# Kernel tuning notes

Measured on AMD Instinct MI355X. Metric: run time of the kernel, lower is better.

Reference implementation:

```python
import jax, jax.numpy as jnp
import numpy as np

N_BASIS = 128   # n_atom_basis F
N_INT   = 3     # n_interactions
N_RBF   = 20
CUTOFF  = 5.0
MAX_Z   = 100
EPS     = 1e-8
N_ATOMS = 25000
N_EDGES = 200000


def setup_inputs() -> dict:
    key = jax.random.key(0)
    ks = jax.random.split(key, 16)
    F = N_BASIS
    s = 0.02
    z     = jax.random.randint(ks[0], (N_ATOMS,), 1, MAX_Z)
    pos   = jax.random.uniform(ks[1], (N_ATOMS, 3), dtype=jnp.float32) * 2.0  # small box -> inside cutoff
    idx_i = jax.random.randint(ks[2], (N_EDGES,), 0, N_ATOMS)
    idx_j = jax.random.randint(ks[3], (N_EDGES,), 0, N_ATOMS)
    emb   = jax.random.normal(ks[4], (MAX_Z, F), dtype=jnp.float32) * s
    fW    = jax.random.normal(ks[5], (N_RBF, 3 * F * N_INT), dtype=jnp.float32) * s
    fb    = jnp.zeros((3 * F * N_INT,), jnp.float32)
    iW1   = jax.random.normal(ks[6], (N_INT, F, F), dtype=jnp.float32) * s
    ib1   = jnp.zeros((N_INT, F), jnp.float32)
    iW2   = jax.random.normal(ks[7], (N_INT, F, 3 * F), dtype=jnp.float32) * s
    ib2   = jnp.zeros((N_INT, 3 * F), jnp.float32)
    mWmix = jax.random.normal(ks[8], (N_INT, F, 2 * F), dtype=jnp.float32) * s
    mW1   = jax.random.normal(ks[9], (N_INT, 2 * F, F), dtype=jnp.float32) * s
    mb1   = jnp.zeros((N_INT, F), jnp.float32)
    mW2   = jax.random.normal(ks[10], (N_INT, F, 3 * F), dtype=jnp.float32) * s
    mb2   = jnp.zeros((N_INT, 3 * F), jnp.float32)
    return dict(z=z, pos=pos, idx_i=idx_i, idx_j=idx_j, emb=emb, fW=fW, fb=fb,
                iW1=iW1, ib1=ib1, iW2=iW2, ib2=ib2,
                mWmix=mWmix, mW1=mW1, mb1=mb1, mW2=mW2, mb2=mb2)


def reference(z, pos, idx_i, idx_j, emb, fW, fb, iW1, ib1, iW2, ib2,
              mWmix, mW1, mb1, mW2, mb2):
    F = N_BASIS
    n_atoms = z.shape[0]
    # geometry
    r_ij = pos[idx_j] - pos[idx_i]                                  # [E,3]
    r_ij = jnp.where(jnp.abs(r_ij) < 1e-6, 1e-6, r_ij)
    d_ij = jnp.linalg.norm(r_ij, axis=1, keepdims=True)             # [E,1]
    dir_ij = r_ij / d_ij                                            # [E,3]
    # Gaussian radial basis
    offsets = jnp.linspace(0.0, CUTOFF, N_RBF)
    width = offsets[1] - offsets[0]
    coeff = -0.5 / (width * width)
    phi = jnp.exp(coeff * (d_ij[..., None] - offsets) ** 2)         # [E,1,n_rbf]
    # cosine cutoff
    fcut = 0.5 * (jnp.cos(jnp.pi * d_ij / CUTOFF) + 1.0) * (d_ij < CUTOFF)  # [E,1]
    filters = (phi @ fW + fb) * fcut[..., None]                     # [E,1,3F*I]
    filter_list = jnp.split(filters, N_INT, axis=-1)                # each [E,1,3F]
    # initial atom features
    q = emb[z][:, None, :]                                          # [N,1,F]
    mu = jnp.zeros((n_atoms, 3, F), q.dtype)                        # [N,3,F]
    for t in range(N_INT):
        # --- interaction (gather - filter-multiply - scatter-add) ---
        x = jax.nn.silu(q @ iW1[t] + ib1[t]) @ iW2[t] + ib2[t]      # [N,1,3F]
        xj = x[idx_j]                                               # [E,1,3F]
        muj = mu[idx_j]                                             # [E,3,F]
        x = filter_list[t] * xj                                     # [E,1,3F]
        dq, dmuR, dmumu = jnp.split(x, 3, axis=-1)                  # [E,1,F] each
        dq = jax.ops.segment_sum(dq, idx_i, num_segments=n_atoms)   # [N,1,F]
        dmu = dmuR * dir_ij[..., None] + dmumu * muj                # [E,3,F]
        dmu = jax.ops.segment_sum(dmu, idx_i, num_segments=n_atoms) # [N,3,F]
        q = q + dq
        mu = mu + dmu
        # --- mixing (intra-atomic) ---
        mu_mix = mu @ mWmix[t]                                      # [N,3,2F]
        mu_V, mu_W = jnp.split(mu_mix, 2, axis=-1)                  # [N,3,F]
        mu_Vn = jnp.sqrt(jnp.sum(mu_V ** 2, axis=-2, keepdims=True) + EPS)  # [N,1,F]
        ctx = jnp.concatenate([q, mu_Vn], axis=-1)                  # [N,1,2F]
        x = jax.nn.silu(ctx @ mW1[t] + mb1[t]) @ mW2[t] + mb2[t]    # [N,1,3F]
        dq_intra, dmu_intra, dqmu_intra = jnp.split(x, 3, axis=-1)
        dmu_intra = dmu_intra * mu_W                                # [N,3,F]
        dqmu_intra = dqmu_intra * jnp.sum(mu_V * mu_W, axis=1, keepdims=True)
        q = q + dq_intra + dqmu_intra
        mu = mu + dmu_intra
    return q.squeeze(1), mu
```

## Files before the change

### kernel.cpp

```cpp
#include <hip/hip_runtime.h>
#include <hip/hip_bf16.h>

#define F 128
#define F3 384
#define NRBF 20
#define NITER 3

typedef __hip_bfloat16 bf16;
typedef __bf16 bfrag __attribute__((ext_vector_type(8)));
typedef float f32x4 __attribute__((ext_vector_type(4)));

__device__ __forceinline__ float b2f(bf16 v) { return __bfloat162float(v); }
__device__ __forceinline__ bf16 f2b(float v) { return __float2bfloat16(v); }
__device__ __forceinline__ bfrag ldb(const bf16* p) { return *(const bfrag*)p; }
__device__ __forceinline__ bfrag ldsb(const __bf16* p) { return *(const bfrag*)p; }
__device__ __forceinline__ bfrag cvtf(const float* p) {
    bfrag r;
#pragma unroll
    for (int j = 0; j < 8; ++j) r[j] = (__bf16)p[j];
    return r;
}

__global__ void detect_kernel(const unsigned short* __restrict__ raw, int n_u16,
                              int* __restrict__ flag) {
    int i = blockIdx.x * blockDim.x + threadIdx.x;
    int bad = 0;
    for (int k = i; k < n_u16; k += blockDim.x * gridDim.x) {
        unsigned e = (raw[k] >> 7) & 0xFFu;
        if (e >= 140u) bad = 1;
    }
    if (bad) atomicOr(flag, 1);
}

__global__ void cvt_dual_kernel(const void* __restrict__ src, float* __restrict__ dst,
                                int n, const int* __restrict__ flag) {
    int i = blockIdx.x * blockDim.x + threadIdx.x;
    if (i >= n) return;
    if (*flag) dst[i] = ((const float*)src)[i];
    else       dst[i] = b2f(((const bf16*)src)[i]);
}

__global__ void transpose_bf16_kernel(const float* __restrict__ src, bf16* __restrict__ dst,
                                      int K, int Nn, int total) {
    int i = blockIdx.x * blockDim.x + threadIdx.x;
    if (i >= total) return;
    int slice = K * Nn;
    int t = i / slice, j = i - t * slice;
    int n = j / K, k = j - n * K;
    dst[i] = f2b(src[t * slice + k * Nn + n]);
}

__global__ void fwt_kernel(const float* __restrict__ fW, const float* __restrict__ fb,
                           bf16* __restrict__ dst, int total) {
    int idx = blockIdx.x * blockDim.x + threadIdx.x;
    if (idx >= total) return;
    int k = idx & 31, rest = idx >> 5;
    int n = rest % F3, t = rest / F3;
    float v = (k < NRBF) ? fW[k * (F3 * NITER) + t * F3 + n]
                         : (k == NRBF ? fb[t * F3 + n] : 0.0f);
    dst[idx] = f2b(v);
}

__global__ void geom_kernel(const float* __restrict__ pos, const int* __restrict__ ii,
                            const int* __restrict__ jj, const int* __restrict__ rank,
                            bf16* __restrict__ phifc2, float* __restrict__ dir2,
                            int* __restrict__ jj2, int E) {
    int e = blockIdx.x * blockDim.x + threadIdx.x;
    if (e >= E) return;
    int i = ii[e], j = jj[e], l = rank[e];
    float r[3];
#pragma unroll
    for (int d = 0; d < 3; ++d) {
        float v = pos[j * 3 + d] - pos[i * 3 + d];
        if (fabsf(v) < 1e-6f) v = 1e-6f;
        r[d] = v;
    }
    float dd = sqrtf(r[0] * r[0] + r[1] * r[1] + r[2] * r[2]);
    float inv = 1.0f / dd;
    jj2[l] = j;
#pragma unroll
    for (int d = 0; d < 3; ++d) dir2[(size_t)l * 4 + d] = r[d] * inv;
    dir2[(size_t)l * 4 + 3] = 0.0f;
    const float CUT = 5.0f;
    const float PI = 3.14159265358979323846f;
    float fc = (dd < CUT) ? 0.5f * (cosf(PI * dd / CUT) + 1.0f) : 0.0f;
    const float width = CUT / (NRBF - 1);
    const float coeff = -0.5f / (width * width);
    bf16* pr = phifc2 + (size_t)l * 32;
#pragma unroll
    for (int k = 0; k < NRBF; ++k) {
        float diff = dd - (float)k * width;
        pr[k] = f2b(expf(coeff * diff * diff) * fc);
    }
    pr[NRBF] = f2b(fc);
#pragma unroll
    for (int k = NRBF + 1; k < 32; ++k) pr[k] = f2b(0.0f);
}

__global__ void embed_kernel(const int* __restrict__ z, const float* __restrict__ emb,
                             float* __restrict__ q, int N) {
    int idx = blockIdx.x * blockDim.x + threadIdx.x;
    if (idx >= N * F) return;
    int n = idx >> 7, f = idx & 127;
    q[idx] = emb[z[n] * F + f];
}

__global__ void count_kernel(const int* __restrict__ ii, int* __restrict__ counts, int E) {
    int e = blockIdx.x * blockDim.x + threadIdx.x;
    if (e < E) atomicAdd(&counts[ii[e]], 1);
}

__global__ void scan_kernel(const int* __restrict__ counts, int* __restrict__ offs, int N) {
    __shared__ int cum[1024];
    int t = threadIdx.x;
    int chunk = (N + 1023) >> 10;
    int b = t * chunk;
    int e = b + chunk; if (e > N) e = N;
    int s = 0;
    for (int a = b; a < e; ++a) s += counts[a];
    cum[t] = s;
    __syncthreads();
    for (int o = 1; o < 1024; o <<= 1) {
        int u = (t >= o) ? cum[t - o] : 0;
        __syncthreads();
        cum[t] += u;
        __syncthreads();
    }
    int run = cum[t] - s;
    for (int a = b; a < e; ++a) { offs[a] = run; run += counts[a]; }
    if (t == 1023) offs[N] = cum[1023];
}

__global__ void fill_kernel(const int* __restrict__ ii, const int* __restrict__ offs,
                            int* __restrict__ cursor, int* __restrict__ rank, int E) {
    int e = blockIdx.x * blockDim.x + threadIdx.x;
    if (e >= E) return;
    int i = ii[e];
    int p = atomicAdd(&cursor[i], 1);
    rank[e] = offs[i] + p;
}

__global__ __launch_bounds__(256) void atom_x_mfma(
    const float* __restrict__ q, const bf16* __restrict__ W1T, const float* __restrict__ b1,
    const bf16* __restrict__ W2T, const float* __restrict__ b2, bf16* __restrict__ x, int N) {
    __shared__ __bf16 H[32][136];
    int tid = threadIdx.x;
    int w = tid >> 6, l = tid & 63;
    int lm = l & 15, q4 = l >> 4;
    int i0 = blockIdx.x * 32;
    f32x4 acc[2][2] = {};
    int r0 = min(i0 + lm, N - 1);
    int r1 = min(i0 + 16 + lm, N - 1);
    for (int kt = 0; kt < 4; ++kt) {
        int ko = kt * 32 + q4 * 8;
        bfrag a0 = cvtf(q + (size_t)r0 * F + ko);
        bfrag a1 = cvtf(q + (size_t)r1 * F + ko);
        bfrag b0 = ldb(W1T + (size_t)(w * 32 + lm) * F + ko);
        bfrag b1f = ldb(W1T + (size_t)(w * 32 + 16 + lm) * F + ko);
        acc[0][0] = __builtin_amdgcn_mfma_f32_16x16x32_bf16(a0, b0, acc[0][0], 0, 0, 0);
        acc[1][0] = __builtin_amdgcn_mfma_f32_16x16x32_bf16(a1, b0, acc[1][0], 0, 0, 0);
        acc[0][1] = __builtin_amdgcn_mfma_f32_16x16x32_bf16(a0, b1f, acc[0][1], 0, 0, 0);
        acc[1][1] = __builtin_amdgcn_mfma_f32_16x16x32_bf16(a1, b1f, acc[1][1], 0, 0, 0);
    }
#pragma unroll
    for (int nt = 0; nt < 2; ++nt) {
        int col = w * 32 + nt * 16 + lm;
        float bb = b1[col];
#pragma unroll
        for (int mt = 0; mt < 2; ++mt)
#pragma unroll
            for (int r = 0; r < 4; ++r) {
                float v = acc[mt][nt][r] + bb;
                H[mt * 16 + q4 * 4 + r][col] = (__bf16)(v / (1.0f + expf(-v)));
            }
    }
    __syncthreads();
#pragma unroll
    for (int j = 0; j < 6; ++j) {
        int n0 = w * 96 + j * 16;
        f32x4 c0 = {}, c1 = {};
        const bf16* bp = W2T + (size_t)(n0 + lm) * F;
        for (int kt = 0; kt < 4; ++kt) {
            int ko = kt * 32 + q4 * 8;
            bfrag a0 = ldsb(&H[lm][ko]);
            bfrag a1 = ldsb(&H[16 + lm][ko]);
            bfrag bf = ldb(bp + ko);
            c0 = __builtin_amdgcn_mfma_f32_16x16x32_bf16(a0, bf, c0, 0, 0, 0);
            c1 = __builtin_amdgcn_mfma_f32_16x16x32_bf16(a1, bf, c1, 0, 0, 0);
        }
        int col = n0 + lm;
        float bb = b2[col];
#pragma unroll
        for (int r = 0; r < 4; ++r) {
            int row0 = i0 + q4 * 4 + r;
            int row1 = row0 + 16;
            if (row0 < N) x[(size_t)row0 * F3 + col] = f2b(c0[r] + bb);
            if (row1 < N) x[(size_t)row1 * F3 + col] = f2b(c1[r] + bb);
        }
    }
}

__global__ __launch_bounds__(384) void edge_gather_mfma(
    float* __restrict__ q, const bf16* __restrict__ mu_in, const bf16* __restrict__ x,
    const bf16* __restrict__ phifc2, const float* __restrict__ dir2,
    const int* __restrict__ jj2, const bf16* __restrict__ fWT,
    const int* __restrict__ offs, bf16* __restrict__ mu_out, int N) {
    __shared__ float filtS[16][393];
    __shared__ float dirS[16][4];
    __shared__ int jjS[16];
    __shared__ float Rs[128][3];
    __shared__ float Ms[128][3];
    int i = blockIdx.x;
    int tid = threadIdx.x;
    int w = tid >> 6, l = tid & 63;
    int lm = l & 15, q4 = l >> 4;
    int beg = offs[i], end = offs[i + 1];
    bfrag Bf[4];
#pragma unroll
    for (int j = 0; j < 4; ++j)
        Bf[j] = ldb(fWT + (size_t)(w * 64 + j * 16 + lm) * 32 + q4 * 8);
    float dq = 0.f;
    float amR0 = 0.f, amR1 = 0.f, amR2 = 0.f;
    float amM0 = 0.f, amM1 = 0.f, amM2 = 0.f;
    for (int c0 = beg; c0 < end; c0 += 16) {
        int cnt = min(16, end - c0);
        if (tid < 16) jjS[tid] = (tid < cnt) ? jj2[c0 + tid] : 0;
        else if (tid >= 64 && tid < 128) {
            int idx = tid - 64;
            int le = idx >> 2, d = idx & 3;
            dirS[le][d] = (le < cnt) ? dir2[(size_t)(c0 + le) * 4 + d] : 0.f;
        }
        bfrag A = ldb(phifc2 + (size_t)(c0 + lm) * 32 + q4 * 8);
        f32x4 C[4] = {};
#pragma unroll
        for (int j = 0; j < 4; ++j)
            C[j] = __builtin_amdgcn_mfma_f32_16x16x32_bf16(A, Bf[j], C[j], 0, 0, 0);
#pragma unroll
        for (int j = 0; j < 4; ++j) {
            int col = w * 64 + j * 16 + lm;
#pragma unroll
            for (int r = 0; r < 4; ++r)
                filtS[q4 * 4 + r][col] = C[j][r];
        }
        __syncthreads();
        if (w < 2) {
            int f = tid;
            for (int le = 0; le < cnt; ++le) {
                int j = jjS[le];
                dq += filtS[le][f] * b2f(x[(size_t)j * F3 + f]);
            }
        } else if (w < 4) {
            int g = tid - 128;
            for (int le = 0; le < cnt; ++le) {
                int j = jjS[le];
                float dR = filtS[le][128 + g] * b2f(x[(size_t)j * F3 + 128 + g]);
                amR0 += dR * dirS[le][0];
                amR1 += dR * dirS[le][1];
                amR2 += dR * dirS[le][2];
            }
        } else {
            int g = tid - 256;
            for (int le = 0; le < cnt; ++le) {
                int j = jjS[le];
                const bf16* mj = mu_in + (size_t)j * F3 + g;
                float dM = filtS[le][256 + g] * b2f(x[(size_t)j * F3 + 256 + g]);
                amM0 += dM * b2f(mj[0]);
                amM1 += dM * b2f(mj[128]);
                amM2 += dM * b2f(mj[256]);
            }
        }
        __syncthreads();
    }
    if (w >= 2 && w < 4) {
        int g = tid - 128;
        Rs[g][0] = amR0; Rs[g][1] = amR1; Rs[g][2] = amR2;
    } else if (w >= 4) {
        int g = tid - 256;
        Ms[g][0] = amM0; Ms[g][1] = amM1; Ms[g][2] = amM2;
    }
    __syncthreads();
    if (tid < 128) {
        int f = tid;
        q[(size_t)i * F + f] += dq;
        size_t mb = (size_t)i * F3 + f;
#pragma unroll
        for (int d = 0; d < 3; ++d)
            mu_out[mb + d * 128] = f2b(b2f(mu_in[mb + d * 128]) + Rs[f][d] + Ms[f][d]);
    }
}

__global__ __launch_bounds__(256) void mix_mfma(
    float* __restrict__ q, bf16* __restrict__ mu,
    const bf16* __restrict__ WmixT, const bf16* __restrict__ W1T, const float* __restrict__ b1,
    const bf16* __restrict__ W2T, const float* __restrict__ b2, int N) {
    __shared__ __bf16 MM[48][264];
    __shared__ __bf16 CT[16][264];
    __shared__ __bf16 HM[16][136];
    __shared__ __bf16 Y[16][392];
    int tid = threadIdx.x;
    int w = tid >> 6, l = tid & 63;
    int lm = l & 15, q4 = l >> 4;
    int i0 = blockIdx.x * 16;
    int rowsM = N * 3;
    {
        f32x4 acc[3][4] = {};
        int mr[3];
#pragma unroll
        for (int mt = 0; mt < 3; ++mt) mr[mt] = min(i0 * 3 + mt * 16 + lm, rowsM - 1);
        for (int kt = 0; kt < 4; ++kt) {
            int ko = kt * 32 + q4 * 8;
            bfrag a[3], b[4];
#pragma unroll
            for (int mt = 0; mt < 3; ++mt) a[mt] = ldb(mu + (size_t)mr[mt] * F + ko);
#pragma unroll
            for (int nt = 0; nt < 4; ++nt)
                b[nt] = ldb(WmixT + (size_t)(w * 64 + nt * 16 + lm) * F + ko);
#pragma unroll
            for (int mt = 0; mt < 3; ++mt)
#pragma unroll
                for (int nt = 0; nt < 4; ++nt)
                    acc[mt][nt] = __builtin_amdgcn_mfma_f32_16x16x32_bf16(a[mt], b[nt], acc[mt][nt], 0, 0, 0);
        }
#pragma unroll
        for (int mt = 0; mt < 3; ++mt)
#pragma unroll
            for (int nt = 0; nt < 4; ++nt)
#pragma unroll
                for (int r = 0; r < 4; ++r)
                    MM[mt * 16 + q4 * 4 + r][w * 64 + nt * 16 + lm] = (__bf16)acc[mt][nt][r];
    }
    __syncthreads();
    for (int idx = tid; idx < 16 * F; idx += 256) {
        int a = idx >> 7, f = idx & 127;
        int i = min(i0 + a, N - 1);
        float v0 = (float)MM[a * 3 + 0][f];
        float v1 = (float)MM[a * 3 + 1][f];
        float v2 = (float)MM[a * 3 + 2][f];
        CT[a][f] = (__bf16)q[(size_t)i * F + f];
        CT[a][F + f] = (__bf16)sqrtf(v0 * v0 + v1 * v1 + v2 * v2 + 1e-8f);
    }
    __syncthreads();
    {
        f32x4 c[2] = {};
        for (int kt = 0; kt < 8; ++kt) {
            int ko = kt * 32 + q4 * 8;
            bfrag a = ldsb(&CT[lm][ko]);
#pragma unroll
            for (int nt = 0; nt < 2; ++nt) {
                bfrag b = ldb(W1T + (size_t)(w * 32 + nt * 16 + lm) * 256 + ko);
                c[nt] = __builtin_amdgcn_mfma_f32_16x16x32_bf16(a, b, c[nt], 0, 0, 0);
            }
        }
#pragma unroll
        for (int nt = 0; nt < 2; ++nt) {
            int col = w * 32 + nt * 16 + lm;
            float bb = b1[col];
#pragma unroll
            for (int r = 0; r < 4; ++r) {
                float v = c[nt][r] + bb;
                HM[q4 * 4 + r][col] = (__bf16)(v / (1.0f + expf(-v)));
            }
        }
    }
    __syncthreads();
#pragma unroll
    for (int j = 0; j < 6; ++j) {
        int n0 = w * 96 + j * 16;
        f32x4 c = {};
        const bf16* bp = W2T + (size_t)(n0 + lm) * F;
        for (int kt = 0; kt < 4; ++kt) {
            int ko = kt * 32 + q4 * 8;
            bfrag a = ldsb(&HM[lm][ko]);
            bfrag b = ldb(bp + ko);
            c = __builtin_amdgcn_mfma_f32_16x16x32_bf16(a, b, c, 0, 0, 0);
        }
        int col = n0 + lm;
        float bb = b2[col];
#pragma unroll
        for (int r = 0; r < 4; ++r)
            Y[q4 * 4 + r][col] = (__bf16)(c[r] + bb);
    }
    __syncthreads();
    for (int idx = tid; idx < 16 * F; idx += 256) {
        int a = idx >> 7, f = idx & 127;
        int i = i0 + a;
        if (i >= N) continue;
        float V0 = (float)MM[a * 3 + 0][f], W0 = (float)MM[a * 3 + 0][F + f];
        float V1 = (float)MM[a * 3 + 1][f], W1v = (float)MM[a * 3 + 1][F + f];
        float V2 = (float)MM[a * 3 + 2][f], W2v = (float)MM[a * 3 + 2][F + f];
        float s = V0 * W0 + V1 * W1v + V2 * W2v;
        float yq = (float)Y[a][f], ym = (float)Y[a][F + f], ys = (float)Y[a][2 * F + f];
        q[(size_t)i * F + f] += yq + ys * s;
        size_t mb = (size_t)i * F3 + f;
        mu[mb]       = f2b(b2f(mu[mb]) + ym * W0);
        mu[mb + 128] = f2b(b2f(mu[mb + 128]) + ym * W1v);
        mu[mb + 256] = f2b(b2f(mu[mb + 256]) + ym * W2v);
    }
}

__global__ void out_kernel(const float* __restrict__ q, const bf16* __restrict__ mu,
                           void* __restrict__ out, int N, const int* __restrict__ flag) {
    int idx = blockIdx.x * blockDim.x + threadIdx.x;
    int nq = N * F;
    int tot = nq + N * F3;
    if (idx >= tot) return;
    float v = (idx < nq) ? q[idx] : b2f(mu[idx - nq]);
    if (*flag) ((float*)out)[idx] = v;
    else       ((bf16*)out)[idx] = f2b(v);
}

extern "C" void kernel_launch(void* const* d_in, const int* in_sizes, int n_in,
                              void* d_out, int out_size, void* d_ws, size_t ws_size,
                              hipStream_t stream) {
    const int* z = (const int*)d_in[0];
    const int* idx_i = (const int*)d_in[2];
    const int* idx_j = (const int*)d_in[3];

    int N = in_sizes[0];
    int E = in_sizes[2];

    char* base = (char*)d_ws;
    size_t off = 0;
    auto alloc = [&](size_t bytes) -> void* {
        void* p = base + off;
        off += (bytes + 255) & ~(size_t)255;
        return p;
    };

    int* flag = (int*)alloc(4);
    float* pos_f = (float*)alloc((size_t)in_sizes[1] * 4);
    float* emb_f = (float*)alloc((size_t)in_sizes[4] * 4);
    float* fW_f = (float*)alloc((size_t)in_sizes[5] * 4);
    float* fb_f = (float*)alloc((size_t)in_sizes[6] * 4);
    float* iW1_f = (float*)alloc((size_t)in_sizes[7] * 4);
    float* ib1_f = (float*)alloc((size_t)in_sizes[8] * 4);
    float* iW2_f = (float*)alloc((size_t)in_sizes[9] * 4);
    float* ib2_f = (float*)alloc((size_t)in_sizes[10] * 4);
    float* mWmix_f = (float*)alloc((size_t)in_sizes[11] * 4);
    float* mW1_f = (float*)alloc((size_t)in_sizes[12] * 4);
    float* mb1_f = (float*)alloc((size_t)in_sizes[13] * 4);
    float* mW2_f = (float*)alloc((size_t)in_sizes[14] * 4);
    float* mb2_f = (float*)alloc((size_t)in_sizes[15] * 4);
    bf16* iW1T = (bf16*)alloc((size_t)NITER * F * F * 2);
    bf16* iW2T = (bf16*)alloc((size_t)NITER * F3 * F * 2);
    bf16* mWmixT = (bf16*)alloc((size_t)NITER * 2 * F * F * 2);
    bf16* mW1T = (bf16*)alloc((size_t)NITER * F * 2 * F * 2);
    bf16* mW2T = (bf16*)alloc((size_t)NITER * F3 * F * 2);
    bf16* fWT = (bf16*)alloc((size_t)NITER * F3 * 32 * 2);
    float* q = (float*)alloc((size_t)N * F * 4);
    bf16* mua = (bf16*)alloc((size_t)N * F3 * 2);
    bf16* mub = (bf16*)alloc((size_t)N * F3 * 2);
    bf16* xbuf = (bf16*)alloc((size_t)N * F3 * 2);
    bf16* phifc2 = (bf16*)alloc((size_t)(E + 16) * 32 * 2);
    float* dir2 = (float*)alloc((size_t)(E + 16) * 4 * 4);
    int* jj2 = (int*)alloc((size_t)(E + 16) * 4);
    int* rank = (int*)alloc((size_t)E * 4);
    int* counts = (int*)alloc((size_t)N * 4);
    int* offs = (int*)alloc((size_t)(N + 1) * 4);

    hipMemsetAsync(flag, 0, 4, stream);
    detect_kernel<<<64, 256, 0, stream>>>((const unsigned short*)d_in[1], in_sizes[1], flag);

    auto cvt = [&](int idx, float* dst) {
        int n = in_sizes[idx];
        cvt_dual_kernel<<<(n + 255) / 256, 256, 0, stream>>>(d_in[idx], dst, n, flag);
    };
    cvt(1, pos_f);
    cvt(4, emb_f);
    cvt(5, fW_f);  cvt(6, fb_f);
    cvt(7, iW1_f); cvt(8, ib1_f);
    cvt(9, iW2_f); cvt(10, ib2_f);
    cvt(11, mWmix_f);
    cvt(12, mW1_f); cvt(13, mb1_f);
    cvt(14, mW2_f); cvt(15, mb2_f);

    auto tpose = [&](const float* src, bf16* dst, int K, int Nn) {
        int total = NITER * K * Nn;
        transpose_bf16_kernel<<<(total + 255) / 256, 256, 0, stream>>>(src, dst, K, Nn, total);
    };
    tpose(iW1_f, iW1T, F, F);
    tpose(iW2_f, iW2T, F, F3);
    tpose(mWmix_f, mWmixT, F, 2 * F);
    tpose(mW1_f, mW1T, 2 * F, F);
    tpose(mW2_f, mW2T, F, F3);
    {
        int total = NITER * F3 * 32;
        fwt_kernel<<<(total + 255) / 256, 256, 0, stream>>>(fW_f, fb_f, fWT, total);
    }

    hipMemsetAsync(counts, 0, (size_t)N * 4, stream);
    count_kernel<<<(E + 255) / 256, 256, 0, stream>>>(idx_i, counts, E);
    scan_kernel<<<1, 1024, 0, stream>>>(counts, offs, N);
    hipMemsetAsync(counts, 0, (size_t)N * 4, stream);
    fill_kernel<<<(E + 255) / 256, 256, 0, stream>>>(idx_i, offs, counts, rank, E);

    geom_kernel<<<(E + 255) / 256, 256, 0, stream>>>(pos_f, idx_i, idx_j, rank,
                                                     phifc2, dir2, jj2, E);
    embed_kernel<<<(N * F + 255) / 256, 256, 0, stream>>>(z, emb_f, q, N);
    hipMemsetAsync(mua, 0, (size_t)N * F3 * 2, stream);

    bf16* muin = mua;
    bf16* muout = mub;
    for (int t = 0; t < NITER; ++t) {
        atom_x_mfma<<<(N + 31) / 32, 256, 0, stream>>>(q, iW1T + (size_t)t * F * F, ib1_f + t * F,
                                                       iW2T + (size_t)t * F3 * F, ib2_f + t * F3,
                                                       xbuf, N);
        edge_gather_mfma<<<N, 384, 0, stream>>>(q, muin, xbuf, phifc2, dir2, jj2,
                                                fWT + (size_t)t * F3 * 32, offs, muout, N);
        mix_mfma<<<(N + 15) / 16, 256, 0, stream>>>(q, muout, mWmixT + (size_t)t * 2 * F * F,
                                                    mW1T + (size_t)t * F * 2 * F, mb1_f + t * F,
                                                    mW2T + (size_t)t * F3 * F, mb2_f + t * F3, N);
        bf16* tm = muin; muin = muout; muout = tm;
    }

    int tot = N * (F + F3);
    out_kernel<<<(tot + 255) / 256, 256, 0, stream>>>(q, muin, d_out, N, flag);
}
```

Baseline: 919.2 us.

## Process 16 atoms per block with segmented edge reduction in edge gather

Result: slower. 1.097 ms (+19.3%).

```diff
diff --git a/kernel.cpp b/kernel.cpp
--- a/kernel.cpp
+++ b/kernel.cpp
@@ -64,7 +64,7 @@
 __global__ void geom_kernel(const float* __restrict__ pos, const int* __restrict__ ii,
                             const int* __restrict__ jj, const int* __restrict__ rank,
                             bf16* __restrict__ phifc2, float* __restrict__ dir2,
-                            int* __restrict__ jj2, int E) {
+                            int* __restrict__ jj2, int* __restrict__ aid2, int E) {
     int e = blockIdx.x * blockDim.x + threadIdx.x;
     if (e >= E) return;
     int i = ii[e], j = jj[e], l = rank[e];
@@ -78,6 +78,7 @@
     float dd = sqrtf(r[0] * r[0] + r[1] * r[1] + r[2] * r[2]);
     float inv = 1.0f / dd;
     jj2[l] = j;
+    aid2[l] = i;
 #pragma unroll
     for (int d = 0; d < 3; ++d) dir2[(size_t)l * 4 + d] = r[d] * inv;
     dir2[(size_t)l * 4 + 3] = 0.0f;
@@ -200,92 +201,95 @@
     }
 }
 
-__global__ __launch_bounds__(384) void edge_gather_mfma(
+__global__ __launch_bounds__(512) void edge_gather_seg(
     float* __restrict__ q, const bf16* __restrict__ mu_in, const bf16* __restrict__ x,
     const bf16* __restrict__ phifc2, const float* __restrict__ dir2,
-    const int* __restrict__ jj2, const bf16* __restrict__ fWT,
-    const int* __restrict__ offs, bf16* __restrict__ mu_out, int N) {
-    __shared__ float filtS[16][393];
-    __shared__ float dirS[16][4];
-    __shared__ int jjS[16];
-    __shared__ float Rs[128][3];
-    __shared__ float Ms[128][3];
-    int i = blockIdx.x;
+    const int* __restrict__ jj2, const int* __restrict__ aid2,
+    const bf16* __restrict__ fWT, const int* __restrict__ offs,
+    bf16* __restrict__ mu_out, int N) {
+    __shared__ float filtS[2][16][396];
+    __shared__ float dirS[2][16][4];
+    __shared__ int jjS[2][16];
+    __shared__ int aidS[2][16];
     int tid = threadIdx.x;
     int w = tid >> 6, l = tid & 63;
     int lm = l & 15, q4 = l >> 4;
-    int beg = offs[i], end = offs[i + 1];
-    bfrag Bf[4];
-#pragma unroll
-    for (int j = 0; j < 4; ++j)
-        Bf[j] = ldb(fWT + (size_t)(w * 64 + j * 16 + lm) * 32 + q4 * 8);
-    float dq = 0.f;
-    float amR0 = 0.f, amR1 = 0.f, amR2 = 0.f;
-    float amM0 = 0.f, amM1 = 0.f, amM2 = 0.f;
-    for (int c0 = beg; c0 < end; c0 += 16) {
+    int a0 = blockIdx.x * 16;
+    int a1 = min(a0 + 16, N);
+    int beg = offs[a0], end = offs[a1];
+    bfrag Bf[3];
+#pragma unroll
+    for (int j = 0; j < 3; ++j)
+        Bf[j] = ldb(fWT + (size_t)(w * 48 + j * 16 + lm) * 32 + q4 * 8);
+    int c = tid >> 7;
+    int f = tid & 127;
+    int d = (c > 0) ? c - 1 : 0;
+    int curA = -1;
+    float acc = 0.0f;
+    int p = 0;
+    for (int c0 = beg; c0 < end; c0 += 16, p ^= 1) {
         int cnt = min(16, end - c0);
-        if (tid < 16) jjS[tid] = (tid < cnt) ? jj2[c0 + tid] : 0;
+        if (tid < 16) jjS[p][tid] = jj2[c0 + tid];
+        else if (tid < 32) aidS[p][tid - 16] = aid2[c0 + tid - 16];
         else if (tid >= 64 && tid < 128) {
             int idx = tid - 64;
-            int le = idx >> 2, d = idx & 3;
-            dirS[le][d] = (le < cnt) ? dir2[(size_t)(c0 + le) * 4 + d] : 0.f;
+            dirS[p][idx >> 2][idx & 3] = dir2[(size_t)(c0 + (idx >> 2)) * 4 + (idx & 3)];
         }
         bfrag A = ldb(phifc2 + (size_t)(c0 + lm) * 32 + q4 * 8);
-        f32x4 C[4] = {};
-#pragma unroll
-        for (int j = 0; j < 4; ++j)
-            C[j] = __builtin_amdgcn_mfma_f32_16x16x32_bf16(A, Bf[j], C[j], 0, 0, 0);
-#pragma unroll
-        for (int j = 0; j < 4; ++j) {
-            int col = w * 64 + j * 16 + lm;
+#pragma unroll
+        for (int j = 0; j < 3; ++j) {
+            f32x4 C = {};
+            C = __builtin_amdgcn_mfma_f32_16x16x32_bf16(A, Bf[j], C, 0, 0, 0);
+            int col = w * 48 + j * 16 + lm;
 #pragma unroll
             for (int r = 0; r < 4; ++r)
-                filtS[q4 * 4 + r][col] = C[j][r];
+                filtS[p][q4 * 4 + r][col] = C[r];
         }
         __syncthreads();
-        if (w < 2) {
-            int f = tid;
+        if (c == 0) {
             for (int le = 0; le < cnt; ++le) {
-                int j = jjS[le];
-                dq += filtS[le][f] * b2f(x[(size_t)j * F3 + f]);
-            }
-        } else if (w < 4) {
-            int g = tid - 128;
-            for (int le = 0; le < cnt; ++le) {
-                int j = jjS[le];
-                float dR = filtS[le][128 + g] * b2f(x[(size_t)j * F3 + 128 + g]);
-                amR0 += dR * dirS[le][0];
-                amR1 += dR * dirS[le][1];
-                amR2 += dR * dirS[le][2];
+                int aid = aidS[p][le];
+                if (aid != curA) {
+                    if (curA >= 0) q[(size_t)curA * F + f] += acc;
+                    curA = aid;
+                    acc = 0.0f;
+                }
+                acc += filtS[p][le][f] * b2f(x[(size_t)jjS[p][le] * F3 + f]);
             }
         } else {
-            int g = tid - 256;
             for (int le = 0; le < cnt; ++le) {
-                int j = jjS[le];
-                const bf16* mj = mu_in + (size_t)j * F3 + g;
-                float dM = filtS[le][256 + g] * b2f(x[(size_t)j * F3 + 256 + g]);
-                amM0 += dM * b2f(mj[0]);
-                amM1 += dM * b2f(mj[128]);
-                amM2 += dM * b2f(mj[256]);
+                int aid = aidS[p][le];
+                if (aid != curA) {
+                    if (curA >= 0) {
+                        size_t mb = (size_t)curA * F3 + d * 128 + f;
+                        mu_out[mb] = f2b(b2f(mu_in[mb]) + acc);
+                    }
+                    curA = aid;
+                    acc = 0.0f;
+                }
+                int j = jjS[p][le];
+                float x1 = b2f(x[(size_t)j * F3 + 128 + f]);
+                float x2 = b2f(x[(size_t)j * F3 + 256 + f]);
+                acc += filtS[p][le][128 + f] * x1 * dirS[p][le][d] +
+                       filtS[p][le][256 + f] * x2 * b2f(mu_in[(size_t)j * F3 + d * 128 + f]);
             }
         }
-        __syncthreads();
-    }
-    if (w >= 2 && w < 4) {
-        int g = tid - 128;
-        Rs[g][0] = amR0; Rs[g][1] = amR1; Rs[g][2] = amR2;
-    } else if (w >= 4) {
-        int g = tid - 256;
-        Ms[g][0] = amM0; Ms[g][1] = amM1; Ms[g][2] = amM2;
-    }
-    __syncthreads();
-    if (tid < 128) {
-        int f = tid;
-        q[(size_t)i * F + f] += dq;
-        size_t mb = (size_t)i * F3 + f;
-#pragma unroll
-        for (int d = 0; d < 3; ++d)
-            mu_out[mb + d * 128] = f2b(b2f(mu_in[mb + d * 128]) + Rs[f][d] + Ms[f][d]);
+    }
+    if (curA >= 0) {
+        if (c == 0) {
+            q[(size_t)curA * F + f] += acc;
+        } else {
+            size_t mb = (size_t)curA * F3 + d * 128 + f;
+            mu_out[mb] = f2b(b2f(mu_in[mb]) + acc);
+        }
+    }
+    if (c >= 1) {
+        for (int a = a0; a < a1; ++a) {
+            if (offs[a] == offs[a + 1]) {
+                size_t mb = (size_t)a * F3 + d * 128 + f;
+                mu_out[mb] = mu_in[mb];
+            }
+        }
     }
 }
 
@@ -454,6 +458,7 @@
     bf16* phifc2 = (bf16*)alloc((size_t)(E + 16) * 32 * 2);
     float* dir2 = (float*)alloc((size_t)(E + 16) * 4 * 4);
     int* jj2 = (int*)alloc((size_t)(E + 16) * 4);
+    int* aid2 = (int*)alloc((size_t)(E + 16) * 4);
     int* rank = (int*)alloc((size_t)E * 4);
     int* counts = (int*)alloc((size_t)N * 4);
     int* offs = (int*)alloc((size_t)(N + 1) * 4);
@@ -495,7 +500,7 @@
     fill_kernel<<<(E + 255) / 256, 256, 0, stream>>>(idx_i, offs, counts, rank, E);
 
     geom_kernel<<<(E + 255) / 256, 256, 0, stream>>>(pos_f, idx_i, idx_j, rank,
-                                                     phifc2, dir2, jj2, E);
+                                                     phifc2, dir2, jj2, aid2, E);
     embed_kernel<<<(N * F + 255) / 256, 256, 0, stream>>>(z, emb_f, q, N);
     hipMemsetAsync(mua, 0, (size_t)N * F3 * 2, stream);
 
@@ -505,8 +510,8 @@
         atom_x_mfma<<<(N + 31) / 32, 256, 0, stream>>>(q, iW1T + (size_t)t * F * F, ib1_f + t * F,
                                                        iW2T + (size_t)t * F3 * F, ib2_f + t * F3,
                                                        xbuf, N);
-        edge_gather_mfma<<<N, 384, 0, stream>>>(q, muin, xbuf, phifc2, dir2, jj2,
-                                                fWT + (size_t)t * F3 * 32, offs, muout, N);
+        edge_gather_seg<<<(N + 15) / 16, 512, 0, stream>>>(q, muin, xbuf, phifc2, dir2, jj2, aid2,
+                                                           fWT + (size_t)t * F3 * 32, offs, muout, N);
         mix_mfma<<<(N + 15) / 16, 256, 0, stream>>>(q, muout, mWmixT + (size_t)t * 2 * F * F,
                                                     mW1T + (size_t)t * F * 2 * F, mb1_f + t * F,
                                                     mW2T + (size_t)t * F3 * F, mb2_f + t * F3, N);
```
